# Performance work log

Hardware: AMD Instinct MI355X
Metric: run time of the kernel (lower is better)

## Reference

```python
import math
import jax, jax.numpy as jnp
import numpy as np

D_MODEL = 1024
N_HEADS = 16
D_K = D_MODEL // N_HEADS
B = 8
L = 1024
LATTICE = (4, 4)
TWO_PI = 2.0 * math.pi


def _build_neighbors():
    """Replicates LatticeMultiHeadAttention._build_neighbors (Moore 8-neighborhood)."""
    positions = [divmod(i, LATTICE[1]) for i in range(N_HEADS)]
    idx = np.full((N_HEADS, 8), -1, dtype=np.int64)
    w = np.zeros((N_HEADS, 8), dtype=np.float32)
    for i, (r1, c1) in enumerate(positions):
        k = 0
        for dr in (-1, 0, 1):
            for dc in (-1, 0, 1):
                if dr == 0 and dc == 0:
                    continue
                if k >= 8:
                    break
                r2, c2 = r1 + dr, c1 + dc
                for j, (r, c) in enumerate(positions):
                    if (r, c) == (r2, c2):
                        idx[i, k] = j
                        w[i, k] = math.exp(-math.hypot(dr, dc))
                        k += 1
                        break
    return idx, w


def setup_inputs() -> dict:
    key = jax.random.key(0)
    ks = jax.random.split(key, 8)
    s = 1.0 / math.sqrt(D_MODEL)
    nbr_idx_np, nbr_w_np = _build_neighbors()
    return {
        "query": jax.random.normal(ks[0], (B, L, D_MODEL), jnp.float32),
        "key_": jax.random.normal(ks[1], (B, L, D_MODEL), jnp.float32),
        "value": jax.random.normal(ks[2], (B, L, D_MODEL), jnp.float32),
        # head-stacked projection weights, stored as [H, d_model, d_k] (x @ W)
        "Wq": jax.random.normal(ks[3], (N_HEADS, D_MODEL, D_K), jnp.float32) * s,
        "Wk": jax.random.normal(ks[4], (N_HEADS, D_MODEL, D_K), jnp.float32) * s,
        "Wv": jax.random.normal(ks[5], (N_HEADS, D_MODEL, D_K), jnp.float32) * s,
        "Wo": jax.random.normal(ks[6], (D_MODEL, D_MODEL), jnp.float32) * s,
        "bo": jax.random.normal(ks[7], (D_MODEL,), jnp.float32) * 0.01,
        # buffers: initial phases (0.0), intrinsic freqs 1 + 0.1*h, lattice tables
        "phases0": jnp.zeros((N_HEADS,), jnp.float32),
        "freqs": jnp.asarray(1.0 + 0.1 * np.arange(N_HEADS), jnp.float32),
        "nbr_w": jnp.asarray(nbr_w_np),
        "nbr_idx": jnp.asarray(nbr_idx_np),
    }


def _updated_phases(phases0, freqs, nbr_w, nbr_idx):
    # multi-head batched Kuramoto step (note: coupling_strength is NOT used here,
    # matching the original forward), then the per-head internal step (empty
    # neighbor_phases branch adds another 0.01 * intrinsic_freq).
    valid = (nbr_idx >= 0).astype(phases0.dtype)        # [H,8]
    nbr_ph = phases0[jnp.clip(nbr_idx, 0, None)] * valid  # [H,8]
    phase_diff = nbr_ph - phases0[:, None]
    force = (nbr_w * jnp.sin(phase_diff)).sum(axis=1)     # [H]
    p1 = jnp.mod(phases0 + 0.01 * (freqs + force), TWO_PI)
    p2 = jnp.mod(p1 + 0.01 * freqs, TWO_PI)
    return p2


def reference(query, key_, value, Wq, Wk, Wv, Wo, bo, phases0, freqs, nbr_w, nbr_idx):
    # phases are torch buffers updated under no_grad -> constants w.r.t. autodiff
    p2 = jax.lax.stop_gradient(
        _updated_phases(phases0, freqs, nbr_w, nbr_idx))
    bias = 0.1 * jnp.cos(p2)                               # [H]

    Q = jnp.einsum('bld,hdk->bhlk', query, Wq)
    K = jnp.einsum('bld,hdk->bhlk', key_, Wk)
    V = jnp.einsum('bld,hdk->bhlk', value, Wv)

    scores = jnp.einsum('bhlk,bhmk->bhlm', Q, K) / jnp.sqrt(
        jnp.asarray(D_K, Q.dtype))
    scores = scores + bias[None, :, None, None]
    attn = jax.nn.softmax(scores, axis=-1)                 # [B,H,L,L]
    ctx = jnp.einsum('bhlm,bhmk->bhlk', attn, V)           # [B,H,L,d_k]
    ctx = ctx.transpose(0, 2, 1, 3).reshape(query.shape[0], query.shape[1], D_MODEL)
    return ctx @ Wo + bo                                   # out_proj
```

## Files before the change

### kernel.cpp

```cpp
#include <hip/hip_runtime.h>
#include <hip/hip_bf16.h>
#include <stdint.h>


typedef unsigned short u16;
typedef __bf16 bf16_t;
typedef bf16_t bf16x8 __attribute__((ext_vector_type(8)));
typedef float f32x4 __attribute__((ext_vector_type(4)));

#define DEVI static __device__ __forceinline__
#define MFMA16(a, b, c) __builtin_amdgcn_mfma_f32_16x16x32_bf16((a), (b), (c), 0, 0, 0)

DEVI void gload_lds16(const void* g, void* l) {
  __builtin_amdgcn_global_load_lds((__attribute__((address_space(1))) void*)g,
                                   (__attribute__((address_space(3))) void*)l, 16, 0, 0);
}

DEVI u16 f2bf(float x) {
  bf16_t b = (bf16_t)x;
  u16 u;
  __builtin_memcpy(&u, &b, 2);
  return u;
}

__global__ __launch_bounds__(256) void prep(const float* __restrict__ Wq,
                                            const float* __restrict__ Wk,
                                            const float* __restrict__ Wv,
                                            const float* __restrict__ Wo,
                                            const float* __restrict__ q,
                                            const float* __restrict__ k,
                                            const float* __restrict__ v,
                                            u16* __restrict__ ws) {
  int bx = blockIdx.x;
  if (bx < 2048) {
    int id = bx * 256 + threadIdx.x;
    int mat = id >> 17;
    int rem = id & 131071;
    const float* src = (mat == 0) ? Wq : (mat == 1) ? Wk : (mat == 2) ? Wv : Wo;
    u16* dst = ws + (size_t)mat * 1048576;
    if (mat < 3) {
      int jb = rem & 7;
      int kk = (rem >> 3) & 1023;
      int h = rem >> 13;
      const float* s = src + h * 65536 + kk * 64 + jb * 8;
      float4 a = *(const float4*)s;
      float4 b = *(const float4*)(s + 4);
      float vv[8] = {a.x, a.y, a.z, a.w, b.x, b.y, b.z, b.w};
#pragma unroll
      for (int jj = 0; jj < 8; jj++)
        dst[(size_t)(h * 64 + jb * 8 + jj) * 1024 + kk] = f2bf(vv[jj]);
    } else {
      int cb = rem & 127;
      int d = rem >> 7;
      const float* s = src + d * 1024 + cb * 8;
      float4 a = *(const float4*)s;
      float4 b = *(const float4*)(s + 4);
      float vv[8] = {a.x, a.y, a.z, a.w, b.x, b.y, b.z, b.w};
#pragma unroll
      for (int jj = 0; jj < 8; jj++)
        dst[(size_t)(cb * 8 + jj) * 1024 + d] = f2bf(vv[jj]);
    }
  } else {
    int id = (bx - 2048) * 256 + threadIdx.x;
    int t = id >> 21;
    size_t rem = (size_t)(id & 2097151) * 4;
    const float* src = (t == 0) ? q : (t == 1) ? k : v;
    float4 a = *(const float4*)(src + rem);
    ushort4 st;
    st.x = f2bf(a.x); st.y = f2bf(a.y); st.z = f2bf(a.z); st.w = f2bf(a.w);
    *(ushort4*)(ws + 4194304 + (size_t)t * 8388608 + rem) = st;
  }
}

__global__ __launch_bounds__(512, 2) void gemm_qkv(const u16* __restrict__ WT,
                                                   const u16* __restrict__ X,
                                                   u16* __restrict__ Qw,
                                                   u16* __restrict__ Kw,
                                                   u16* __restrict__ Vw) {
  __shared__ __align__(1024) u16 lds[65536];
  int tid = threadIdx.x;
  int wid = tid >> 6, lane = tid & 63, quad = lane >> 4, l16 = lane & 15;
  int wm = wid >> 2, wn = wid & 3;

  int orig = blockIdx.x;
  int wgid = (orig & 7) * 48 + (orig >> 3);
  int z = wgid >> 7;
  int rr = wgid & 127;
  int nt0 = rr >> 2, mt0 = rr & 3;
  const u16* Ag = WT + (size_t)z * 1048576;
  const u16* Bg = X + (size_t)z * 8388608;
  u16* out = (z == 0) ? Qw : (z == 1) ? Kw : Vw;
  float oscale = (z == 0) ? 0.125f : 1.0f;
  int m0 = mt0 << 8, n0 = nt0 << 8;

  const u16* gA = Ag + (size_t)m0 * 1024;
  const u16* gB = Bg + (size_t)n0 * 1024;
  int rA = tid >> 3;
  int lc = (tid & 7) ^ (rA & 7);
  size_t goff = (size_t)rA * 1024 + lc * 8;

  char* ldsc = (char*)lds;
  int rx = l16 & 7;
  int baA = wm * 16384;
  int baB = (2 + (wn >> 1)) * 16384 + (wn & 1) * 8192;

  auto stageA = [&](int buf, int half, int kt) {
    const u16* g = gA + (size_t)(half * 128) * 1024 + kt * 64 + goff;
    char* d = ldsc + (buf * 4 + half) * 16384 + wid * 1024;
    gload_lds16(g, d);
    gload_lds16(g + 65536, d + 8192);
  };
  auto stageB = [&](int buf, int half, int kt) {
    const u16* g = gB + (size_t)(half * 128) * 1024 + kt * 64 + goff;
    char* d = ldsc + (buf * 4 + 2 + half) * 16384 + wid * 1024;
    gload_lds16(g, d);
    gload_lds16(g + 65536, d + 8192);
  };
  auto rdA = [&](int buf, int mh, int mf, int ks) -> bf16x8 {
    return *(const bf16x8*)(ldsc + (buf << 16) + baA + (mh * 64 + mf * 16 + l16) * 128 +
                            ((((ks << 2) | quad) ^ rx) << 4));
  };
  auto rdB = [&](int buf, int nf, int ks) -> bf16x8 {
    return *(const bf16x8*)(ldsc + (buf << 16) + baB + (nf * 16 + l16) * 128 +
                            ((((ks << 2) | quad) ^ rx) << 4));
  };

  f32x4 acc[8][4];
#pragma unroll
  for (int i = 0; i < 8; ++i)
#pragma unroll
    for (int j = 0; j < 4; ++j) acc[i][j] = {0.f, 0.f, 0.f, 0.f};
  bf16x8 af[4][2], bfr[4][2];

  stageA(0, 0, 0); stageA(0, 1, 0);
  stageB(0, 0, 0); stageB(0, 1, 0);
  stageB(1, 0, 1); stageB(1, 1, 1);
  asm volatile("s_waitcnt vmcnt(4)" ::: "memory");
  __builtin_amdgcn_s_barrier();

  for (int t = 0; t < 16; ++t) {
    int cur = t & 1, nxt = cur ^ 1;

#pragma unroll
    for (int mf = 0; mf < 4; ++mf)
#pragma unroll
      for (int ks = 0; ks < 2; ++ks) af[mf][ks] = rdA(cur, 0, mf, ks);
#pragma unroll
    for (int nf = 0; nf < 2; ++nf)
#pragma unroll
      for (int ks = 0; ks < 2; ++ks) bfr[nf][ks] = rdB(cur, nf, ks);
    if (t < 15) stageA(nxt, 0, t + 1);
    __builtin_amdgcn_s_barrier();
    __builtin_amdgcn_s_setprio(1);
#pragma unroll
    for (int ks = 0; ks < 2; ++ks)
#pragma unroll
      for (int mf = 0; mf < 4; ++mf)
#pragma unroll
        for (int nf = 0; nf < 2; ++nf)
          acc[mf][nf] = MFMA16(af[mf][ks], bfr[nf][ks], acc[mf][nf]);
    __builtin_amdgcn_s_setprio(0);
    __builtin_amdgcn_s_barrier();

#pragma unroll
    for (int nf = 2; nf < 4; ++nf)
#pragma unroll
      for (int ks = 0; ks < 2; ++ks) bfr[nf][ks] = rdB(cur, nf, ks);
    if (t < 15) stageA(nxt, 1, t + 1);
    __builtin_amdgcn_s_barrier();
    __builtin_amdgcn_s_setprio(1);
#pragma unroll
    for (int ks = 0; ks < 2; ++ks)
#pragma unroll
      for (int mf = 0; mf < 4; ++mf)
#pragma unroll
        for (int nf = 2; nf < 4; ++nf)
          acc[mf][nf] = MFMA16(af[mf][ks], bfr[nf][ks], acc[mf][nf]);
    __builtin_amdgcn_s_setprio(0);
    __builtin_amdgcn_s_barrier();

#pragma unroll
    for (int mf = 0; mf < 4; ++mf)
#pragma unroll
      for (int ks = 0; ks < 2; ++ks) af[mf][ks] = rdA(cur, 1, mf, ks);
    if (t < 14) stageB(cur, 0, t + 2);
    __builtin_amdgcn_s_barrier();
    __builtin_amdgcn_s_setprio(1);
#pragma unroll
    for (int ks = 0; ks < 2; ++ks)
#pragma unroll
      for (int mf = 0; mf < 4; ++mf)
#pragma unroll
        for (int nf = 2; nf < 4; ++nf)
          acc[4 + mf][nf] = MFMA16(af[mf][ks], bfr[nf][ks], acc[4 + mf][nf]);
    __builtin_amdgcn_s_setprio(0);
    __builtin_amdgcn_s_barrier();

    if (t < 14) stageB(cur, 1, t + 2);
    __builtin_amdgcn_s_barrier();
    __builtin_amdgcn_s_setprio(1);
#pragma unroll
    for (int ks = 0; ks < 2; ++ks)
#pragma unroll
      for (int mf = 0; mf < 4; ++mf)
#pragma unroll
        for (int nf = 0; nf < 2; ++nf)
          acc[4 + mf][nf] = MFMA16(af[mf][ks], bfr[nf][ks], acc[4 + mf][nf]);
    __builtin_amdgcn_s_setprio(0);
    asm volatile("s_waitcnt vmcnt(4)" ::: "memory");
    __builtin_amdgcn_s_barrier();
  }

#pragma unroll
  for (int mfg = 0; mfg < 8; ++mfg) {
    int m = m0 + wm * 128 + mfg * 16 + quad * 4;
    int h = m >> 6, dk = m & 63;
#pragma unroll
    for (int nf = 0; nf < 4; ++nf) {
      int n = n0 + wn * 64 + nf * 16 + l16;
      int bb = n >> 10, l = n & 1023;
      f32x4 v = acc[mfg][nf];
      if (z < 2) {
        ushort4 st;
        st.x = f2bf(v[0] * oscale); st.y = f2bf(v[1] * oscale);
        st.z = f2bf(v[2] * oscale); st.w = f2bf(v[3] * oscale);
        *(ushort4*)(out + ((size_t)((bb * 16 + h) * 1024 + l) * 64 + dk)) = st;
      } else {
        size_t base = ((size_t)((bb * 16 + h) * 64 + dk)) * 1024 + l;
        out[base] = f2bf(v[0]);
        out[base + 1024] = f2bf(v[1]);
        out[base + 2048] = f2bf(v[2]);
        out[base + 3072] = f2bf(v[3]);
      }
    }
  }
}

__global__ __launch_bounds__(256) void gemm_out(const u16* __restrict__ A,
                                                const u16* __restrict__ Bx,
                                                float* __restrict__ outf,
                                                const float* __restrict__ bias) {
  __shared__ __align__(16) u16 sA[128 * 32];
  __shared__ __align__(16) u16 sB[128 * 32];
  int id = blockIdx.x + 8 * blockIdx.y;
  int xcd = id & 7, j = id >> 3;
  int mtile = j & 7;
  int nt = xcd * 8 + (j >> 3);
  int tid = threadIdx.x;
  int wid = tid >> 6, lane = tid & 63, quad = lane >> 4, l16 = lane & 15;
  int wm = wid >> 1, wn = wid & 1;
  int m0 = mtile * 128, n0 = nt * 128;

  f32x4 acc[4][4];
#pragma unroll
  for (int i = 0; i < 4; i++)
#pragma unroll
    for (int jj = 0; jj < 4; jj++) acc[i][jj] = {0.f, 0.f, 0.f, 0.f};

  for (int k0 = 0; k0 < 1024; k0 += 32) {
#pragma unroll
    for (int p = 0; p < 2; p++) {
      int cl = p * 256 + tid;
      int r = cl >> 2, kc = cl & 3;
      gload_lds16(A + (size_t)(m0 + r) * 1024 + k0 + kc * 8,
                  (char*)sA + (p * 256 + wid * 64) * 16);
      gload_lds16(Bx + (size_t)(n0 + r) * 1024 + k0 + kc * 8,
                  (char*)sB + (p * 256 + wid * 64) * 16);
    }
    __syncthreads();
    bf16x8 af[4], bfr[4];
#pragma unroll
    for (int mt = 0; mt < 4; mt++)
      af[mt] = *(const bf16x8*)((const char*)sA + ((wm * 64 + mt * 16 + l16) * 64 + quad * 16));
#pragma unroll
    for (int ntf = 0; ntf < 4; ntf++)
      bfr[ntf] = *(const bf16x8*)((const char*)sB + ((wn * 64 + ntf * 16 + l16) * 64 + quad * 16));
#pragma unroll
    for (int mt = 0; mt < 4; mt++)
#pragma unroll
      for (int ntf = 0; ntf < 4; ntf++) acc[mt][ntf] = MFMA16(af[mt], bfr[ntf], acc[mt][ntf]);
    __syncthreads();
  }

#pragma unroll
  for (int mt = 0; mt < 4; mt++) {
    int m = m0 + wm * 64 + mt * 16 + quad * 4;
#pragma unroll
    for (int ntf = 0; ntf < 4; ntf++) {
      int n = n0 + wn * 64 + ntf * 16 + l16;
      f32x4 v = acc[mt][ntf];
      float4 st;
      st.x = v[0] + bias[m];
      st.y = v[1] + bias[m + 1];
      st.z = v[2] + bias[m + 2];
      st.w = v[3] + bias[m + 3];
      *(float4*)(outf + ((size_t)n * 1024 + m)) = st;
    }
  }
}

__global__ __launch_bounds__(256, 4) void attn_k(const u16* __restrict__ Q,
                                                 const u16* __restrict__ K,
                                                 const u16* __restrict__ VT,
                                                 u16* __restrict__ CTX) {
  __shared__ __align__(16) u16 sQ[128 * 64];
  __shared__ __align__(16) u16 sK[64 * 64];
  __shared__ __align__(16) u16 sV[64 * 64];
  int tid = threadIdx.x;
  int wid = tid >> 6, lane = tid & 63, quad = lane >> 4, l16 = lane & 15;
  int id = blockIdx.x + 8 * blockIdx.y;
  int xcd = id & 7, j = id >> 3;
  int qt = j & 7;
  int bh = xcd * 16 + (j >> 3);
  const u16* Qb = Q + (size_t)bh * 65536;
  const u16* Kb = K + (size_t)bh * 65536;
  const u16* Vb = VT + (size_t)bh * 65536;
  int q0 = qt * 128;

#pragma unroll
  for (int p = 0; p < 4; p++) {
    int cl = p * 256 + tid;
    int r = cl >> 3, c = cl & 7, g = c ^ (r & 7);
    gload_lds16(Qb + (size_t)(q0 + r) * 64 + g * 8, (char*)sQ + (p * 256 + wid * 64) * 16);
  }
  __syncthreads();

  bf16x8 bq[2][2];
#pragma unroll
  for (int qf = 0; qf < 2; qf++) {
    int row = wid * 32 + qf * 16 + l16;
#pragma unroll
    for (int ks = 0; ks < 2; ks++) {
      int ch = (ks * 4 + quad) ^ (row & 7);
      bq[qf][ks] = *(const bf16x8*)((const char*)sQ + row * 128 + ch * 16);
    }
  }

  u16* sPw = sQ + wid * 2048;

  f32x4 oacc[4][2];
#pragma unroll
  for (int i = 0; i < 4; i++) {
    oacc[i][0] = {0.f, 0.f, 0.f, 0.f};
    oacc[i][1] = {0.f, 0.f, 0.f, 0.f};
  }
  float lsum[2] = {0.f, 0.f};

  for (int lk0 = 0; lk0 < 1024; lk0 += 64) {
#pragma unroll
    for (int p = 0; p < 2; p++) {
      int cl = p * 256 + tid;
      int r = cl >> 3, c = cl & 7, g = c ^ (r & 7);
      gload_lds16(Kb + (size_t)(lk0 + r) * 64 + g * 8, (char*)sK + (p * 256 + wid * 64) * 16);
      gload_lds16(Vb + (size_t)r * 1024 + lk0 + g * 8, (char*)sV + (p * 256 + wid * 64) * 16);
    }
    __syncthreads();

    f32x4 s[4][2];
#pragma unroll
    for (int mt = 0; mt < 4; mt++) {
      s[mt][0] = {0.f, 0.f, 0.f, 0.f};
      s[mt][1] = {0.f, 0.f, 0.f, 0.f};
    }
#pragma unroll
    for (int ks = 0; ks < 2; ks++) {
#pragma unroll
      for (int mt = 0; mt < 4; mt++) {
        int row = mt * 16 + l16;
        int ch = (ks * 4 + quad) ^ (row & 7);
        bf16x8 a = *(const bf16x8*)((const char*)sK + row * 128 + ch * 16);
        s[mt][0] = MFMA16(a, bq[0][ks], s[mt][0]);
        s[mt][1] = MFMA16(a, bq[1][ks], s[mt][1]);
      }
    }

#pragma unroll
    for (int qf = 0; qf < 2; qf++) {
      int row = qf * 16 + l16;
#pragma unroll
      for (int mt = 0; mt < 4; mt++) {
        float p0 = __expf(s[mt][qf][0]);
        float p1 = __expf(s[mt][qf][1]);
        float p2 = __expf(s[mt][qf][2]);
        float p3 = __expf(s[mt][qf][3]);
        lsum[qf] += (p0 + p1) + (p2 + p3);
        ushort4 st;
        st.x = f2bf(p0); st.y = f2bf(p1); st.z = f2bf(p2); st.w = f2bf(p3);
        int ch = (2 * mt + (quad >> 1)) ^ (row & 7);
        *(ushort4*)((char*)sPw + row * 128 + ch * 16 + (quad & 1) * 8) = st;
      }
    }
    asm volatile("s_waitcnt lgkmcnt(0)" ::: "memory");

    bf16x8 bp[2][2];
#pragma unroll
    for (int qf = 0; qf < 2; qf++) {
      int row = qf * 16 + l16;
#pragma unroll
      for (int c = 0; c < 2; c++) {
        int ch = (c * 4 + quad) ^ (row & 7);
        bp[qf][c] = *(const bf16x8*)((const char*)sPw + row * 128 + ch * 16);
      }
    }
#pragma unroll
    for (int c = 0; c < 2; c++) {
#pragma unroll
      for (int mt = 0; mt < 4; mt++) {
        int row = mt * 16 + l16;
        int ch = (c * 4 + quad) ^ (row & 7);
        bf16x8 a = *(const bf16x8*)((const char*)sV + row * 128 + ch * 16);
        oacc[mt][0] = MFMA16(a, bp[0][c], oacc[mt][0]);
        oacc[mt][1] = MFMA16(a, bp[1][c], oacc[mt][1]);
      }
    }
    __syncthreads();
  }

#pragma unroll
  for (int qf = 0; qf < 2; qf++) {
    lsum[qf] += __shfl_xor(lsum[qf], 16, 64);
    lsum[qf] += __shfl_xor(lsum[qf], 32, 64);
  }
  float inv0 = 1.f / lsum[0], inv1 = 1.f / lsum[1];

  int b = bh >> 4, h = bh & 15;
#pragma unroll
  for (int qf = 0; qf < 2; qf++) {
    int qg = q0 + wid * 32 + qf * 16 + l16;
    float inv = qf ? inv1 : inv0;
#pragma unroll
    for (int mt = 0; mt < 4; mt++) {
      int dk = mt * 16 + quad * 4;
      ushort4 st;
      st.x = f2bf(oacc[mt][qf][0] * inv);
      st.y = f2bf(oacc[mt][qf][1] * inv);
      st.z = f2bf(oacc[mt][qf][2] * inv);
      st.w = f2bf(oacc[mt][qf][3] * inv);
      *(ushort4*)(CTX + (((size_t)(b * 1024 + qg) * 16 + h) * 64 + dk)) = st;
    }
  }
}

extern "C" void kernel_launch(void* const* d_in, const int* in_sizes, int n_in,
                              void* d_out, int out_size, void* d_ws, size_t ws_size,
                              hipStream_t stream) {
  (void)in_sizes; (void)n_in; (void)out_size;
  const float* query = (const float*)d_in[0];
  const float* key_ = (const float*)d_in[1];
  const float* value = (const float*)d_in[2];
  const float* Wq = (const float*)d_in[3];
  const float* Wk = (const float*)d_in[4];
  const float* Wv = (const float*)d_in[5];
  const float* Wo = (const float*)d_in[6];
  const float* bo = (const float*)d_in[7];

  u16* ws = (u16*)d_ws;
  u16* WT = ws;
  u16* X = ws + 4194304;
  u16* Qw = ws + 29360128;
  u16* Kw = ws + 37748736;
  u16* Vw = ws + 46137344;
  u16* Cw = X;
  float* outp = (float*)d_out;

  prep<<<26624, 256, 0, stream>>>(Wq, Wk, Wv, Wo, query, key_, value, ws);
  gemm_qkv<<<dim3(384), 512, 0, stream>>>(WT, X, Qw, Kw, Vw);
  attn_k<<<dim3(8, 128), 256, 0, stream>>>(Qw, Kw, Vw, Cw);
  gemm_out<<<dim3(8, 64), 256, 0, stream>>>(WT + 3145728, Cw, outp, bo);
}
```

Measured before the change: 309.6 us.

## Retile QKV GEMM to 128x128, pipeline out-proj GEMM, LDS-transpose weight prep

The QKV projection GEMM moves from 512-thread 256x256 tiles to 256-thread 128x128 tiles with a double-buffered, two-stage-ahead direct-to-LDS pipeline and a swizzled layout, giving four times as many workgroups. The output projection GEMM adopts the same pipelined structure with K-step 64 in place of its unpipelined 32-wide loop, and loads the bias as a vector. The weight-prep kernel now transposes through a shared-memory tile so both global reads and bf16 writes are coalesced, replacing the strided scalar stores. Smaller QKV tiles lower reuse per block in exchange for better occupancy and load balance across CUs.

```diff
diff --git a/kernel.cpp b/kernel.cpp
--- a/kernel.cpp
+++ b/kernel.cpp
@@ -6,6 +6,7 @@
 typedef unsigned short u16;
 typedef __bf16 bf16_t;
 typedef bf16_t bf16x8 __attribute__((ext_vector_type(8)));
+typedef u16 u16x8 __attribute__((ext_vector_type(8)));
 typedef float f32x4 __attribute__((ext_vector_type(4)));
 
 #define DEVI static __device__ __forceinline__
@@ -32,36 +33,36 @@
                                             const float* __restrict__ v,
                                             u16* __restrict__ ws) {
   int bx = blockIdx.x;
-  if (bx < 2048) {
-    int id = bx * 256 + threadIdx.x;
-    int mat = id >> 17;
-    int rem = id & 131071;
+  if (bx < 1024) {
+    __shared__ float T[64][65];
+    int mat = bx >> 8, ti = bx & 255;
+    int rb = ti >> 4, cb = ti & 15;
     const float* src = (mat == 0) ? Wq : (mat == 1) ? Wk : (mat == 2) ? Wv : Wo;
     u16* dst = ws + (size_t)mat * 1048576;
-    if (mat < 3) {
-      int jb = rem & 7;
-      int kk = (rem >> 3) & 1023;
-      int h = rem >> 13;
-      const float* s = src + h * 65536 + kk * 64 + jb * 8;
-      float4 a = *(const float4*)s;
-      float4 b = *(const float4*)(s + 4);
-      float vv[8] = {a.x, a.y, a.z, a.w, b.x, b.y, b.z, b.w};
-#pragma unroll
-      for (int jj = 0; jj < 8; jj++)
-        dst[(size_t)(h * 64 + jb * 8 + jj) * 1024 + kk] = f2bf(vv[jj]);
-    } else {
-      int cb = rem & 127;
-      int d = rem >> 7;
-      const float* s = src + d * 1024 + cb * 8;
-      float4 a = *(const float4*)s;
-      float4 b = *(const float4*)(s + 4);
-      float vv[8] = {a.x, a.y, a.z, a.w, b.x, b.y, b.z, b.w};
-#pragma unroll
-      for (int jj = 0; jj < 8; jj++)
-        dst[(size_t)(cb * 8 + jj) * 1024 + d] = f2bf(vv[jj]);
+    int stride = (mat < 3) ? 64 : 1024;
+    size_t srcBase = (mat < 3) ? ((size_t)rb * 65536 + cb * 4096)
+                               : ((size_t)rb * 65536 + cb * 64);
+    size_t dstBase = (mat < 3) ? ((size_t)rb * 65536 + cb * 64)
+                               : ((size_t)cb * 65536 + rb * 64);
+#pragma unroll
+    for (int p = 0; p < 4; ++p) {
+      int e = p * 256 + threadIdx.x;
+      int rr = e >> 4, c4 = (e & 15) * 4;
+      float4 vv = *(const float4*)(src + srcBase + (size_t)rr * stride + c4);
+      T[rr][c4] = vv.x; T[rr][c4 + 1] = vv.y; T[rr][c4 + 2] = vv.z; T[rr][c4 + 3] = vv.w;
+    }
+    __syncthreads();
+#pragma unroll
+    for (int p = 0; p < 2; ++p) {
+      int e = p * 256 + threadIdx.x;
+      int n = e >> 3, c8 = (e & 7) * 8;
+      u16x8 o;
+#pragma unroll
+      for (int i = 0; i < 8; ++i) o[i] = f2bf(T[c8 + i][n]);
+      *(u16x8*)(dst + dstBase + (size_t)n * 1024 + c8) = o;
     }
   } else {
-    int id = (bx - 2048) * 256 + threadIdx.x;
+    int id = (bx - 1024) * 256 + threadIdx.x;
     int t = id >> 21;
     size_t rem = (size_t)(id & 2097151) * 4;
     const float* src = (t == 0) ? q : (t == 1) ? k : v;
@@ -72,228 +73,218 @@
   }
 }
 
-__global__ __launch_bounds__(512, 2) void gemm_qkv(const u16* __restrict__ WT,
+__global__ __launch_bounds__(256, 2) void gemm_qkv(const u16* __restrict__ WT,
                                                    const u16* __restrict__ X,
                                                    u16* __restrict__ Qw,
                                                    u16* __restrict__ Kw,
                                                    u16* __restrict__ Vw) {
-  __shared__ __align__(1024) u16 lds[65536];
+  __shared__ __align__(1024) u16 lds[2][2][8192];
+  char* ldsc = (char*)lds;
   int tid = threadIdx.x;
   int wid = tid >> 6, lane = tid & 63, quad = lane >> 4, l16 = lane & 15;
-  int wm = wid >> 2, wn = wid & 3;
-
-  int orig = blockIdx.x;
-  int wgid = (orig & 7) * 48 + (orig >> 3);
-  int z = wgid >> 7;
-  int rr = wgid & 127;
-  int nt0 = rr >> 2, mt0 = rr & 3;
-  const u16* Ag = WT + (size_t)z * 1048576;
-  const u16* Bg = X + (size_t)z * 8388608;
+  int wm = wid >> 1, wn = wid & 1;
+
+  int id = blockIdx.x;
+  int wgid = (id & 7) * 192 + (id >> 3);
+  int mt = wgid & 7;
+  int rest = wgid >> 3;
+  int nt = rest & 63;
+  int z = rest >> 6;
+  const u16* Ag = WT + (size_t)z * 1048576 + (size_t)mt * 131072;
+  const u16* Bg = X + (size_t)z * 8388608 + (size_t)nt * 131072;
   u16* out = (z == 0) ? Qw : (z == 1) ? Kw : Vw;
   float oscale = (z == 0) ? 0.125f : 1.0f;
-  int m0 = mt0 << 8, n0 = nt0 << 8;
-
-  const u16* gA = Ag + (size_t)m0 * 1024;
-  const u16* gB = Bg + (size_t)n0 * 1024;
-  int rA = tid >> 3;
-  int lc = (tid & 7) ^ (rA & 7);
-  size_t goff = (size_t)rA * 1024 + lc * 8;
-
-  char* ldsc = (char*)lds;
+
+  int r0 = tid >> 3;
+  int lc = (tid ^ r0) & 7;
+  size_t gbase = (size_t)r0 * 1024 + lc * 8;
+
   int rx = l16 & 7;
-  int baA = wm * 16384;
-  int baB = (2 + (wn >> 1)) * 16384 + (wn & 1) * 8192;
-
-  auto stageA = [&](int buf, int half, int kt) {
-    const u16* g = gA + (size_t)(half * 128) * 1024 + kt * 64 + goff;
-    char* d = ldsc + (buf * 4 + half) * 16384 + wid * 1024;
-    gload_lds16(g, d);
-    gload_lds16(g + 65536, d + 8192);
-  };
-  auto stageB = [&](int buf, int half, int kt) {
-    const u16* g = gB + (size_t)(half * 128) * 1024 + kt * 64 + goff;
-    char* d = ldsc + (buf * 4 + 2 + half) * 16384 + wid * 1024;
-    gload_lds16(g, d);
-    gload_lds16(g + 65536, d + 8192);
-  };
-  auto rdA = [&](int buf, int mh, int mf, int ks) -> bf16x8 {
-    return *(const bf16x8*)(ldsc + (buf << 16) + baA + (mh * 64 + mf * 16 + l16) * 128 +
+  int rowA = wm * 64 + l16;
+  int rowB = wn * 64 + l16;
+
+  auto stage = [&](int buf, int kt) {
+#pragma unroll
+    for (int p = 0; p < 4; ++p)
+      gload_lds16(Ag + gbase + (size_t)p * 32768 + kt * 64,
+                  ldsc + buf * 32768 + p * 4096 + tid * 16);
+#pragma unroll
+    for (int p = 0; p < 4; ++p)
+      gload_lds16(Bg + gbase + (size_t)p * 32768 + kt * 64,
+                  ldsc + buf * 32768 + 16384 + p * 4096 + tid * 16);
+  };
+  auto rdA = [&](int buf, int mf, int ks) -> bf16x8 {
+    return *(const bf16x8*)(ldsc + buf * 32768 + (rowA + mf * 16) * 128 +
                             ((((ks << 2) | quad) ^ rx) << 4));
   };
   auto rdB = [&](int buf, int nf, int ks) -> bf16x8 {
-    return *(const bf16x8*)(ldsc + (buf << 16) + baB + (nf * 16 + l16) * 128 +
+    return *(const bf16x8*)(ldsc + buf * 32768 + 16384 + (rowB + nf * 16) * 128 +
                             ((((ks << 2) | quad) ^ rx) << 4));
   };
 
-  f32x4 acc[8][4];
-#pragma unroll
-  for (int i = 0; i < 8; ++i)
+  f32x4 acc[4][4];
+#pragma unroll
+  for (int i = 0; i < 4; ++i)
 #pragma unroll
     for (int j = 0; j < 4; ++j) acc[i][j] = {0.f, 0.f, 0.f, 0.f};
   bf16x8 af[4][2], bfr[4][2];
 
-  stageA(0, 0, 0); stageA(0, 1, 0);
-  stageB(0, 0, 0); stageB(0, 1, 0);
-  stageB(1, 0, 1); stageB(1, 1, 1);
-  asm volatile("s_waitcnt vmcnt(4)" ::: "memory");
+  stage(0, 0);
+  stage(1, 1);
+  asm volatile("s_waitcnt vmcnt(8)" ::: "memory");
   __builtin_amdgcn_s_barrier();
 
   for (int t = 0; t < 16; ++t) {
-    int cur = t & 1, nxt = cur ^ 1;
-
+    int cur = t & 1;
 #pragma unroll
     for (int mf = 0; mf < 4; ++mf)
 #pragma unroll
-      for (int ks = 0; ks < 2; ++ks) af[mf][ks] = rdA(cur, 0, mf, ks);
-#pragma unroll
-    for (int nf = 0; nf < 2; ++nf)
+      for (int ks = 0; ks < 2; ++ks) af[mf][ks] = rdA(cur, mf, ks);
+#pragma unroll
+    for (int nf = 0; nf < 4; ++nf)
 #pragma unroll
       for (int ks = 0; ks < 2; ++ks) bfr[nf][ks] = rdB(cur, nf, ks);
-    if (t < 15) stageA(nxt, 0, t + 1);
+    asm volatile("s_waitcnt lgkmcnt(0)" ::: "memory");
     __builtin_amdgcn_s_barrier();
+    if (t < 14) stage(cur, t + 2);
     __builtin_amdgcn_s_setprio(1);
 #pragma unroll
     for (int ks = 0; ks < 2; ++ks)
 #pragma unroll
       for (int mf = 0; mf < 4; ++mf)
 #pragma unroll
-        for (int nf = 0; nf < 2; ++nf)
+        for (int nf = 0; nf < 4; ++nf)
           acc[mf][nf] = MFMA16(af[mf][ks], bfr[nf][ks], acc[mf][nf]);
     __builtin_amdgcn_s_setprio(0);
+    if (t < 14)
+      asm volatile("s_waitcnt vmcnt(8)" ::: "memory");
+    else
+      asm volatile("s_waitcnt vmcnt(0)" ::: "memory");
     __builtin_amdgcn_s_barrier();
-
-#pragma unroll
-    for (int nf = 2; nf < 4; ++nf)
-#pragma unroll
-      for (int ks = 0; ks < 2; ++ks) bfr[nf][ks] = rdB(cur, nf, ks);
-    if (t < 15) stageA(nxt, 1, t + 1);
-    __builtin_amdgcn_s_barrier();
-    __builtin_amdgcn_s_setprio(1);
-#pragma unroll
-    for (int ks = 0; ks < 2; ++ks)
-#pragma unroll
-      for (int mf = 0; mf < 4; ++mf)
-#pragma unroll
-        for (int nf = 2; nf < 4; ++nf)
-          acc[mf][nf] = MFMA16(af[mf][ks], bfr[nf][ks], acc[mf][nf]);
-    __builtin_amdgcn_s_setprio(0);
-    __builtin_amdgcn_s_barrier();
-
-#pragma unroll
-    for (int mf = 0; mf < 4; ++mf)
-#pragma unroll
-      for (int ks = 0; ks < 2; ++ks) af[mf][ks] = rdA(cur, 1, mf, ks);
-    if (t < 14) stageB(cur, 0, t + 2);
-    __builtin_amdgcn_s_barrier();
-    __builtin_amdgcn_s_setprio(1);
-#pragma unroll
-    for (int ks = 0; ks < 2; ++ks)
-#pragma unroll
-      for (int mf = 0; mf < 4; ++mf)
-#pragma unroll
-        for (int nf = 2; nf < 4; ++nf)
-          acc[4 + mf][nf] = MFMA16(af[mf][ks], bfr[nf][ks], acc[4 + mf][nf]);
-    __builtin_amdgcn_s_setprio(0);
-    __builtin_amdgcn_s_barrier();
-
-    if (t < 14) stageB(cur, 1, t + 2);
-    __builtin_amdgcn_s_barrier();
-    __builtin_amdgcn_s_setprio(1);
-#pragma unroll
-    for (int ks = 0; ks < 2; ++ks)
-#pragma unroll
-      for (int mf = 0; mf < 4; ++mf)
-#pragma unroll
-        for (int nf = 0; nf < 2; ++nf)
-          acc[4 + mf][nf] = MFMA16(af[mf][ks], bfr[nf][ks], acc[4 + mf][nf]);
-    __builtin_amdgcn_s_setprio(0);
-    asm volatile("s_waitcnt vmcnt(4)" ::: "memory");
-    __builtin_amdgcn_s_barrier();
-  }
-
-#pragma unroll
-  for (int mfg = 0; mfg < 8; ++mfg) {
-    int m = m0 + wm * 128 + mfg * 16 + quad * 4;
+  }
+
+#pragma unroll
+  for (int mf = 0; mf < 4; ++mf) {
+    int m = mt * 128 + wm * 64 + mf * 16 + quad * 4;
     int h = m >> 6, dk = m & 63;
 #pragma unroll
     for (int nf = 0; nf < 4; ++nf) {
-      int n = n0 + wn * 64 + nf * 16 + l16;
+      int n = nt * 128 + wn * 64 + nf * 16 + l16;
       int bb = n >> 10, l = n & 1023;
-      f32x4 v = acc[mfg][nf];
+      f32x4 vv = acc[mf][nf];
       if (z < 2) {
         ushort4 st;
-        st.x = f2bf(v[0] * oscale); st.y = f2bf(v[1] * oscale);
-        st.z = f2bf(v[2] * oscale); st.w = f2bf(v[3] * oscale);
+        st.x = f2bf(vv[0] * oscale); st.y = f2bf(vv[1] * oscale);
+        st.z = f2bf(vv[2] * oscale); st.w = f2bf(vv[3] * oscale);
         *(ushort4*)(out + ((size_t)((bb * 16 + h) * 1024 + l) * 64 + dk)) = st;
       } else {
         size_t base = ((size_t)((bb * 16 + h) * 64 + dk)) * 1024 + l;
-        out[base] = f2bf(v[0]);
-        out[base + 1024] = f2bf(v[1]);
-        out[base + 2048] = f2bf(v[2]);
-        out[base + 3072] = f2bf(v[3]);
+        out[base] = f2bf(vv[0]);
+        out[base + 1024] = f2bf(vv[1]);
+        out[base + 2048] = f2bf(vv[2]);
+        out[base + 3072] = f2bf(vv[3]);
       }
     }
   }
 }
 
-__global__ __launch_bounds__(256) void gemm_out(const u16* __restrict__ A,
-                                                const u16* __restrict__ Bx,
-                                                float* __restrict__ outf,
-                                                const float* __restrict__ bias) {
-  __shared__ __align__(16) u16 sA[128 * 32];
-  __shared__ __align__(16) u16 sB[128 * 32];
-  int id = blockIdx.x + 8 * blockIdx.y;
-  int xcd = id & 7, j = id >> 3;
-  int mtile = j & 7;
-  int nt = xcd * 8 + (j >> 3);
+__global__ __launch_bounds__(256, 2) void gemm_out(const u16* __restrict__ A,
+                                                   const u16* __restrict__ Bx,
+                                                   float* __restrict__ outf,
+                                                   const float* __restrict__ bias) {
+  __shared__ __align__(1024) u16 lds[2][2][8192];
+  char* ldsc = (char*)lds;
   int tid = threadIdx.x;
   int wid = tid >> 6, lane = tid & 63, quad = lane >> 4, l16 = lane & 15;
   int wm = wid >> 1, wn = wid & 1;
-  int m0 = mtile * 128, n0 = nt * 128;
+
+  int id = blockIdx.x;
+  int wgid = (id & 7) * 64 + (id >> 3);
+  int mt = wgid & 7;
+  int nt = wgid >> 3;
+  const u16* Ag = A + (size_t)mt * 131072;
+  const u16* Bg = Bx + (size_t)nt * 131072;
+
+  int r0 = tid >> 3;
+  int lc = (tid ^ r0) & 7;
+  size_t gbase = (size_t)r0 * 1024 + lc * 8;
+  int rx = l16 & 7;
+  int rowA = wm * 64 + l16;
+  int rowB = wn * 64 + l16;
+
+  auto stage = [&](int buf, int kt) {
+#pragma unroll
+    for (int p = 0; p < 4; ++p)
+      gload_lds16(Ag + gbase + (size_t)p * 32768 + kt * 64,
+                  ldsc + buf * 32768 + p * 4096 + tid * 16);
+#pragma unroll
+    for (int p = 0; p < 4; ++p)
+      gload_lds16(Bg + gbase + (size_t)p * 32768 + kt * 64,
+                  ldsc + buf * 32768 + 16384 + p * 4096 + tid * 16);
+  };
+  auto rdA = [&](int buf, int mf, int ks) -> bf16x8 {
+    return *(const bf16x8*)(ldsc + buf * 32768 + (rowA + mf * 16) * 128 +
+                            ((((ks << 2) | quad) ^ rx) << 4));
+  };
+  auto rdB = [&](int buf, int nf, int ks) -> bf16x8 {
+    return *(const bf16x8*)(ldsc + buf * 32768 + 16384 + (rowB + nf * 16) * 128 +
+                            ((((ks << 2) | quad) ^ rx) << 4));
+  };
 
   f32x4 acc[4][4];
 #pragma unroll
-  for (int i = 0; i < 4; i++)
-#pragma unroll
-    for (int jj = 0; jj < 4; jj++) acc[i][jj] = {0.f, 0.f, 0.f, 0.f};
-
-  for (int k0 = 0; k0 < 1024; k0 += 32) {
-#pragma unroll
-    for (int p = 0; p < 2; p++) {
-      int cl = p * 256 + tid;
-      int r = cl >> 2, kc = cl & 3;
-      gload_lds16(A + (size_t)(m0 + r) * 1024 + k0 + kc * 8,
-                  (char*)sA + (p * 256 + wid * 64) * 16);
-      gload_lds16(Bx + (size_t)(n0 + r) * 1024 + k0 + kc * 8,
-                  (char*)sB + (p * 256 + wid * 64) * 16);
-    }
-    __syncthreads();
-    bf16x8 af[4], bfr[4];
-#pragma unroll
-    for (int mt = 0; mt < 4; mt++)
-      af[mt] = *(const bf16x8*)((const char*)sA + ((wm * 64 + mt * 16 + l16) * 64 + quad * 16));
-#pragma unroll
-    for (int ntf = 0; ntf < 4; ntf++)
-      bfr[ntf] = *(const bf16x8*)((const char*)sB + ((wn * 64 + ntf * 16 + l16) * 64 + quad * 16));
-#pragma unroll
-    for (int mt = 0; mt < 4; mt++)
-#pragma unroll
-      for (int ntf = 0; ntf < 4; ntf++) acc[mt][ntf] = MFMA16(af[mt], bfr[ntf], acc[mt][ntf]);
-    __syncthreads();
-  }
-
-#pragma unroll
-  for (int mt = 0; mt < 4; mt++) {
-    int m = m0 + wm * 64 + mt * 16 + quad * 4;
-#pragma unroll
-    for (int ntf = 0; ntf < 4; ntf++) {
-      int n = n0 + wn * 64 + ntf * 16 + l16;
-      f32x4 v = acc[mt][ntf];
+  for (int i = 0; i < 4; ++i)
+#pragma unroll
+    for (int j = 0; j < 4; ++j) acc[i][j] = {0.f, 0.f, 0.f, 0.f};
+  bf16x8 af[4][2], bfr[4][2];
+
+  stage(0, 0);
+  stage(1, 1);
+  asm volatile("s_waitcnt vmcnt(8)" ::: "memory");
+  __builtin_amdgcn_s_barrier();
+
+  for (int t = 0; t < 16; ++t) {
+    int cur = t & 1;
+#pragma unroll
+    for (int mf = 0; mf < 4; ++mf)
+#pragma unroll
+      for (int ks = 0; ks < 2; ++ks) af[mf][ks] = rdA(cur, mf, ks);
+#pragma unroll
+    for (int nf = 0; nf < 4; ++nf)
+#pragma unroll
+      for (int ks = 0; ks < 2; ++ks) bfr[nf][ks] = rdB(cur, nf, ks);
+    asm volatile("s_waitcnt lgkmcnt(0)" ::: "memory");
+    __builtin_amdgcn_s_barrier();
+    if (t < 14) stage(cur, t + 2);
+    __builtin_amdgcn_s_setprio(1);
+#pragma unroll
+    for (int ks = 0; ks < 2; ++ks)
+#pragma unroll
+      for (int mf = 0; mf < 4; ++mf)
+#pragma unroll
+        for (int nf = 0; nf < 4; ++nf)
+          acc[mf][nf] = MFMA16(af[mf][ks], bfr[nf][ks], acc[mf][nf]);
+    __builtin_amdgcn_s_setprio(0);
+    if (t < 14)
+      asm volatile("s_waitcnt vmcnt(8)" ::: "memory");
+    else
+      asm volatile("s_waitcnt vmcnt(0)" ::: "memory");
+    __builtin_amdgcn_s_barrier();
+  }
+
+#pragma unroll
+  for (int mf = 0; mf < 4; ++mf) {
+    int m = mt * 128 + wm * 64 + mf * 16 + quad * 4;
+    float4 bq = *(const float4*)(bias + m);
+#pragma unroll
+    for (int nf = 0; nf < 4; ++nf) {
+      int n = nt * 128 + wn * 64 + nf * 16 + l16;
+      f32x4 vv = acc[mf][nf];
       float4 st;
-      st.x = v[0] + bias[m];
-      st.y = v[1] + bias[m + 1];
-      st.z = v[2] + bias[m + 2];
-      st.w = v[3] + bias[m + 3];
+      st.x = vv[0] + bq.x;
+      st.y = vv[1] + bq.y;
+      st.z = vv[2] + bq.z;
+      st.w = vv[3] + bq.w;
       *(float4*)(outf + ((size_t)n * 1024 + m)) = st;
     }
   }
@@ -463,8 +454,8 @@
   u16* Cw = X;
   float* outp = (float*)d_out;
 
-  prep<<<26624, 256, 0, stream>>>(Wq, Wk, Wv, Wo, query, key_, value, ws);
-  gemm_qkv<<<dim3(384), 512, 0, stream>>>(WT, X, Qw, Kw, Vw);
+  prep<<<25600, 256, 0, stream>>>(Wq, Wk, Wv, Wo, query, key_, value, ws);
+  gemm_qkv<<<dim3(1536), 256, 0, stream>>>(WT, X, Qw, Kw, Vw);
   attn_k<<<dim3(8, 128), 256, 0, stream>>>(Qw, Kw, Vw, Cw);
-  gemm_out<<<dim3(8, 64), 256, 0, stream>>>(WT + 3145728, Cw, outp, bo);
-}
+  gemm_out<<<dim3(512), 256, 0, stream>>>(WT + 3145728, Cw, outp, bo);
+}
```

Measured after the change: 277.6 us. 1.12x faster.
